# Kernel tuning notes

Measured on AMD Instinct MI355X. Metric: run time of the kernel, lower is better.

The kernel has to match this reference:

```python
import jax, jax.numpy as jnp
import numpy as np

HID = 64

def setup_inputs() -> dict:
    key = jax.random.key(0)
    ks = jax.random.split(key, 32)
    Nc, Na, B = 65536, 8192, 128
    Ecc, Eca, Eac, Eaa = 1048576, 262144, 262144, 131072
    d = {}
    d['x_context'] = jax.random.normal(ks[0], (Nc, 2), jnp.float32)
    d['x_action'] = jax.random.normal(ks[1], (Na, 2), jnp.float32)
    d['timestep'] = jax.random.randint(ks[2], (B,), 0, 1000)
    d['batch_idx'] = jax.random.randint(ks[3], (Na,), 0, B)
    d['cc_src'] = jax.random.randint(ks[4], (Ecc,), 0, Nc)
    d['cc_dst'] = jax.random.randint(ks[5], (Ecc,), 0, Nc)
    d['ca_src'] = jax.random.randint(ks[6], (Eca,), 0, Nc)
    d['ca_dst'] = jax.random.randint(ks[7], (Eca,), 0, Na)
    d['ac_src'] = jax.random.randint(ks[8], (Eac,), 0, Na)
    d['ac_dst'] = jax.random.randint(ks[9], (Eac,), 0, Nc)
    d['aa_src'] = jax.random.randint(ks[10], (Eaa,), 0, Na)
    d['aa_dst'] = jax.random.randint(ks[11], (Eaa,), 0, Na)
    def w(k, shape, fan_in):
        return jax.random.normal(k, shape, jnp.float32) / np.sqrt(fan_in)
    # input embeddings
    d['W_ctx'] = w(ks[12], (2, HID), 2); d['b_ctx'] = jnp.zeros((HID,), jnp.float32)
    d['W_act'] = w(ks[13], (2, HID), 2); d['b_act'] = jnp.zeros((HID,), jnp.float32)
    # time MLP
    d['tW1'] = w(ks[14], (HID, 2 * HID), HID); d['tb1'] = jnp.zeros((2 * HID,), jnp.float32)
    d['tW2'] = w(ks[15], (2 * HID, HID), 2 * HID); d['tb2'] = jnp.zeros((HID,), jnp.float32)
    # 2 SAGE layers, 4 edge types each (stacked: [cc, ca, ac, aa])
    d['c1_Wl'] = w(ks[16], (4, HID, HID), HID); d['c1_bl'] = jnp.zeros((4, HID), jnp.float32)
    d['c1_Wr'] = w(ks[17], (4, HID, HID), HID)
    d['c2_Wl'] = w(ks[18], (4, HID, HID), HID); d['c2_bl'] = jnp.zeros((4, HID), jnp.float32)
    d['c2_Wr'] = w(ks[19], (4, HID, HID), HID)
    # noise predictor
    d['nW1'] = w(ks[20], (2 * HID, HID), 2 * HID); d['nb1'] = jnp.zeros((HID,), jnp.float32)
    d['nW2'] = w(ks[21], (HID, 2), HID); d['nb2'] = jnp.zeros((2,), jnp.float32)
    return d


def _sage(x_src, x_dst, src, dst, Wl, bl, Wr):
    # PyG SAGEConv: lin_l(mean of neighbor msgs) + lin_r(self)
    n_dst = x_dst.shape[0]
    s = jax.ops.segment_sum(x_src[src], dst, num_segments=n_dst)
    cnt = jax.ops.segment_sum(jnp.ones((src.shape[0], 1), x_src.dtype), dst, num_segments=n_dst)
    mean = s / jnp.maximum(cnt, 1.0)
    return mean @ Wl + bl + x_dst @ Wr


def reference(x_context, x_action, timestep, batch_idx, cc_src, cc_dst, ca_src, ca_dst, ac_src, ac_dst, aa_src, aa_dst, W_ctx, b_ctx, W_act, b_act, tW1, tb1, tW2, tb2, c1_Wl, c1_bl, c1_Wr, c2_Wl, c2_bl, c2_Wr, nW1, nb1, nW2, nb2):
    h_ctx = x_context @ W_ctx + b_ctx           # [Nc, H]
    h_act = x_action @ W_act + b_act            # [Na, H]
    # hetero SAGE layer 1 (aggr='sum' over edge types per dst node type)
    o_ctx = (_sage(h_ctx, h_ctx, cc_src, cc_dst, c1_Wl[0], c1_bl[0], c1_Wr[0])
             + _sage(h_act, h_ctx, ac_src, ac_dst, c1_Wl[2], c1_bl[2], c1_Wr[2]))
    o_act = (_sage(h_ctx, h_act, ca_src, ca_dst, c1_Wl[1], c1_bl[1], c1_Wr[1])
             + _sage(h_act, h_act, aa_src, aa_dst, c1_Wl[3], c1_bl[3], c1_Wr[3]))
    h_ctx, h_act = jax.nn.relu(o_ctx), jax.nn.relu(o_act)
    # hetero SAGE layer 2
    o_act = (_sage(h_ctx, h_act, ca_src, ca_dst, c2_Wl[1], c2_bl[1], c2_Wr[1])
             + _sage(h_act, h_act, aa_src, aa_dst, c2_Wl[3], c2_bl[3], c2_Wr[3]))
    action_features = o_act                      # [Na, H]
    # sinusoidal time embedding + MLP
    half = HID // 2
    freqs = jnp.exp(-jnp.log(10000.0) * jnp.arange(half, dtype=jnp.float32) / (half - 1))
    ang = timestep.astype(jnp.float32)[:, None] * freqs[None, :]
    temb = jnp.concatenate([jnp.sin(ang), jnp.cos(ang)], axis=-1)   # [B, H]
    temb = jax.nn.gelu(temb @ tW1 + tb1, approximate=False) @ tW2 + tb2
    # gather per-node time embedding, fuse, predict noise
    fused = jnp.concatenate([action_features, temb[batch_idx]], axis=-1)  # [Na, 2H]
    h = jax.nn.gelu(fused @ nW1 + nb1, approximate=False)
    return h @ nW2 + nb2                         # [Na, node_features]
```

## Files before the change

### kernel.cpp

```cpp
#include <hip/hip_runtime.h>
#include <math.h>

#define HID 64
#define SLOTS 8192
#define WCC 40
#define WAC 10
#define NSCAT 64
#define CAP_CA 112
#define CAP_AA 80

__device__ __forceinline__ float gelu_exact(float x) {
    return 0.5f * x * (1.0f + erff(x * 0.70710678118654752f));
}

__device__ __forceinline__ float bf2f(unsigned short u) {
    return __uint_as_float(((unsigned int)u) << 16);
}
__device__ __forceinline__ unsigned short f2bf(float x) {
    unsigned int b = __float_as_uint(x);
    b += 0x7FFFu + ((b >> 16) & 1u);
    return (unsigned short)(b >> 16);
}

#define FXS 32768.0f
#define FXB (1 << 19)

__device__ __forceinline__ unsigned long long pack_edge(float2 v) {
    unsigned int f0 = (unsigned int)(__float2int_rn(v.x * FXS) + FXB);
    unsigned int f1 = (unsigned int)(__float2int_rn(v.y * FXS) + FXB);
    return (1ULL << 52) | ((unsigned long long)f1 << 26) | f0;
}

__device__ __forceinline__ void decode_acc(unsigned long long A, float& s0, float& s1, float& c) {
    int cnt = (int)(A >> 52);
    long long f0 = (long long)(A & 0x3FFFFFFULL) - (long long)cnt * FXB;
    long long f1 = (long long)((A >> 26) & 0x3FFFFFFULL) - (long long)cnt * FXB;
    s0 = (float)f0 * (1.0f / FXS);
    s1 = (float)f1 * (1.0f / FXS);
    c = (float)cnt;
}

__global__ __launch_bounds__(1024) void mega_kernel(
    const float* __restrict__ W_ctx, const float* __restrict__ b_ctx,
    const float* __restrict__ W_act, const float* __restrict__ b_act,
    const float* __restrict__ c1_Wl, const float* __restrict__ c1_bl,
    const float* __restrict__ c1_Wr,
    const float* __restrict__ c2_Wr, const float* __restrict__ c2_bl,
    float* __restrict__ P,
    const int* __restrict__ timestep,
    const float* __restrict__ tW1, const float* __restrict__ tb1,
    const float* __restrict__ tW2, const float* __restrict__ tb2,
    float* __restrict__ temb, int B,
    const int* __restrict__ cc_src, const int* __restrict__ cc_dst,
    const float* __restrict__ x_ctx, unsigned long long* __restrict__ pcc,
    int Ecc, int perCC,
    const int* __restrict__ ac_src, const int* __restrict__ ac_dst,
    const float* __restrict__ x_act, unsigned long long* __restrict__ pac,
    int Eac, int perAC,
    const int* __restrict__ ca_src, const int* __restrict__ ca_dst, int Eca,
    const int* __restrict__ aa_src, const int* __restrict__ aa_dst, int Eaa,
    int* __restrict__ cur_ca, int* __restrict__ csr_ca,
    int* __restrict__ cur_aa, int* __restrict__ csr_aa,
    int Nc, int bCC, int bAC, int bSC) {
    __shared__ unsigned long long slab[SLOTS];
    int blk = blockIdx.x;
    int tid = threadIdx.x;

    if (blk == 0) {
        if (tid < 64) {
            int j = tid;
            float a0, a1, c;

            a0 = a1 = c = 0.f;
            for (int k = 0; k < 64; k++) {
                float l = c1_Wr[k * 64 + j] + c1_Wr[2 * 4096 + k * 64 + j];
                a0 += W_ctx[k] * l; a1 += W_ctx[64 + k] * l; c += b_ctx[k] * l;
            }
            P[j] = a0; P[64 + j] = a1; P[128 + j] = c + c1_bl[j] + c1_bl[128 + j];

            a0 = a1 = c = 0.f;
            for (int k = 0; k < 64; k++) {
                float l = c1_Wl[k * 64 + j];
                a0 += W_ctx[k] * l; a1 += W_ctx[64 + k] * l; c += b_ctx[k] * l;
            }
            P[192 + j] = a0; P[256 + j] = a1; P[320 + j] = c;

            a0 = a1 = c = 0.f;
            for (int k = 0; k < 64; k++) {
                float l = c1_Wl[2 * 4096 + k * 64 + j];
                a0 += W_act[k] * l; a1 += W_act[64 + k] * l; c += b_act[k] * l;
            }
            P[384 + j] = a0; P[448 + j] = a1; P[512 + j] = c;

            a0 = a1 = c = 0.f;
            for (int k = 0; k < 64; k++) {
                float l = c1_Wr[4096 + k * 64 + j] + c1_Wr[3 * 4096 + k * 64 + j];
                a0 += W_act[k] * l; a1 += W_act[64 + k] * l; c += b_act[k] * l;
            }
            P[576 + j] = a0; P[640 + j] = a1; P[704 + j] = c + c1_bl[64 + j] + c1_bl[192 + j];

            a0 = a1 = c = 0.f;
            for (int k = 0; k < 64; k++) {
                float l = c1_Wl[4096 + k * 64 + j];
                a0 += W_ctx[k] * l; a1 += W_ctx[64 + k] * l; c += b_ctx[k] * l;
            }
            P[768 + j] = a0; P[832 + j] = a1; P[896 + j] = c;

            a0 = a1 = c = 0.f;
            for (int k = 0; k < 64; k++) {
                float l = c1_Wl[3 * 4096 + k * 64 + j];
                a0 += W_act[k] * l; a1 += W_act[64 + k] * l; c += b_act[k] * l;
            }
            P[960 + j] = a0; P[1024 + j] = a1; P[1088 + j] = c;

            for (int k = 0; k < 64; k++)
                P[1152 + k * 64 + j] = c2_Wr[4096 + k * 64 + j] + c2_Wr[3 * 4096 + k * 64 + j];
            P[5248 + j] = c2_bl[64 + j] + c2_bl[192 + j];
        }
    } else if (blk < bCC) {
        float* fl = (float*)slab;
        int sub = tid >> 7;
        int t = tid & 127;
        int b = (blk - 1) * 8 + sub;
        bool vb = (b < B);
        float* e = fl + sub * 64;
        float* t1 = fl + 512 + sub * 128;
        float ts = vb ? (float)timestep[b] : 0.f;
        if (t < 64) {
            int jj = t & 31;
            float f = expf(-9.210340371976184f * (float)jj / 31.0f);
            float ang = ts * f;
            e[t] = (t < 32) ? sinf(ang) : cosf(ang);
        }
        __syncthreads();
        {
            float a = tb1[t];
            #pragma unroll 8
            for (int k = 0; k < 64; k++) a += e[k] * tW1[k * 128 + t];
            t1[t] = gelu_exact(a);
        }
        __syncthreads();
        if (t < 64 && vb) {
            float a = tb2[t];
            #pragma unroll 8
            for (int k = 0; k < 128; k++) a += t1[k] * tW2[k * 64 + t];
            temb[b * 64 + t] = a;
        }
    } else if (blk < bAC) {
        int q = blk - bCC;
        int r = q / WCC, s = q % WCC;
        for (int k = tid; k < SLOTS; k += 1024) slab[k] = 0;
        __syncthreads();
        int lo = r * SLOTS;
        int e0 = s * perCC;
        int e1 = min(e0 + perCC, Ecc);
        const float2* xc2 = (const float2*)x_ctx;
        for (int e = e0 + tid * 4; e < e1; e += 4096) {
            int4 d4 = *(const int4*)(cc_dst + e);
            int4 s4 = *(const int4*)(cc_src + e);
            unsigned int o0 = (unsigned int)(d4.x - lo);
            unsigned int o1 = (unsigned int)(d4.y - lo);
            unsigned int o2 = (unsigned int)(d4.z - lo);
            unsigned int o3 = (unsigned int)(d4.w - lo);
            if (o0 < SLOTS) atomicAdd(&slab[o0], pack_edge(xc2[s4.x]));
            if (o1 < SLOTS) atomicAdd(&slab[o1], pack_edge(xc2[s4.y]));
            if (o2 < SLOTS) atomicAdd(&slab[o2], pack_edge(xc2[s4.z]));
            if (o3 < SLOTS) atomicAdd(&slab[o3], pack_edge(xc2[s4.w]));
        }
        __syncthreads();
        for (int k = tid; k < SLOTS; k += 1024)
            pcc[(size_t)s * Nc + lo + k] = slab[k];
    } else if (blk < bSC) {
        int q = blk - bAC;
        int r = q / WAC, s = q % WAC;
        for (int k = tid; k < SLOTS; k += 1024) slab[k] = 0;
        __syncthreads();
        int lo = r * SLOTS;
        int e0 = s * perAC;
        int e1 = min(e0 + perAC, Eac);
        const float2* xa2 = (const float2*)x_act;
        for (int e = e0 + tid * 4; e < e1; e += 4096) {
            int4 d4 = *(const int4*)(ac_dst + e);
            int4 s4 = *(const int4*)(ac_src + e);
            unsigned int o0 = (unsigned int)(d4.x - lo);
            unsigned int o1 = (unsigned int)(d4.y - lo);
            unsigned int o2 = (unsigned int)(d4.z - lo);
            unsigned int o3 = (unsigned int)(d4.w - lo);
            if (o0 < SLOTS) atomicAdd(&slab[o0], pack_edge(xa2[s4.x]));
            if (o1 < SLOTS) atomicAdd(&slab[o1], pack_edge(xa2[s4.y]));
            if (o2 < SLOTS) atomicAdd(&slab[o2], pack_edge(xa2[s4.z]));
            if (o3 < SLOTS) atomicAdd(&slab[o3], pack_edge(xa2[s4.w]));
        }
        __syncthreads();
        for (int k = tid; k < SLOTS; k += 1024)
            pac[(size_t)s * Nc + lo + k] = slab[k];
    } else {
        int tot = Eca + Eaa;
        for (int e = (blk - bSC) * 1024 + tid; e < tot; e += NSCAT * 1024) {
            if (e < Eca) {
                int d = ca_dst[e];
                int pos = atomicAdd(&cur_ca[d], 1);
                if (pos < CAP_CA) csr_ca[d * CAP_CA + pos] = ca_src[e];
            } else {
                int e2 = e - Eca;
                int d = aa_dst[e2];
                int pos = atomicAdd(&cur_aa[d], 1);
                if (pos < CAP_AA) csr_aa[d * CAP_AA + pos] = aa_src[e2];
            }
        }
    }
}

__global__ void mid_kernel(const unsigned long long* __restrict__ pcc,
                           const unsigned long long* __restrict__ pac,
                           const float* __restrict__ x_ctx, const float* __restrict__ x_act,
                           const float* __restrict__ P,
                           const int* __restrict__ cur_ca, const int* __restrict__ csr_ca,
                           const int* __restrict__ cur_aa, const int* __restrict__ csr_aa,
                           unsigned short* __restrict__ hb_ctx,
                           unsigned short* __restrict__ hb_act,
                           int Nc, int Na, int Gctx) {
    int blk = blockIdx.x;
    if (blk < Gctx) {
        __shared__ float nd[256][8];
        int t = threadIdx.x;
        int i = blk * 256 + t;
        if (i < Nc) {
            unsigned long long A = 0, Bv = 0;
            #pragma unroll
            for (int s = 0; s < WCC; s++) A += pcc[(size_t)s * Nc + i];
            #pragma unroll
            for (int s = 0; s < WAC; s++) Bv += pac[(size_t)s * Nc + i];
            float s0, s1, cc, a0, a1, ca;
            decode_acc(A, s0, s1, cc);
            decode_acc(Bv, a0, a1, ca);
            float2 xv = ((const float2*)x_ctx)[i];
            float rcc = 1.f / fmaxf(cc, 1.f), rac = 1.f / fmaxf(ca, 1.f);
            nd[t][0] = s0 * rcc; nd[t][1] = s1 * rcc; nd[t][2] = (cc > 0.f) ? 1.f : 0.f;
            nd[t][3] = a0 * rac; nd[t][4] = a1 * rac; nd[t][5] = (ca > 0.f) ? 1.f : 0.f;
            nd[t][6] = xv.x; nd[t][7] = xv.y;
        }
        __syncthreads();
        int t2 = threadIdx.x;
        int ns = t2 >> 6, j = t2 & 63;
        float p0 = P[j], p1 = P[64 + j], p2 = P[128 + j];
        float p3 = P[192 + j], p4 = P[256 + j], p5 = P[320 + j];
        float p6 = P[384 + j], p7 = P[448 + j], p8 = P[512 + j];
        for (int it = 0; it < 64; it++) {
            int ln = it * 4 + ns;
            int gi = blk * 256 + ln;
            if (gi >= Nc) break;
            float o = nd[ln][6] * p0 + nd[ln][7] * p1 + p2
                    + nd[ln][0] * p3 + nd[ln][1] * p4 + nd[ln][2] * p5
                    + nd[ln][3] * p6 + nd[ln][4] * p7 + nd[ln][5] * p8;
            hb_ctx[(size_t)gi * 64 + j] = f2bf(fmaxf(o, 0.f));
        }
    } else {
        int n = threadIdx.x >> 6, lane = threadIdx.x & 63;
        int i = (blk - Gctx) * 4 + n;
        if (i >= Na) return;
        const float2* xc2 = (const float2*)x_ctx;
        const float2* xa2 = (const float2*)x_act;
        int m_ca = cur_ca[i], it_ca = min(m_ca, CAP_CA);
        int b0 = i * CAP_CA;
        float s0 = 0.f, s1 = 0.f;
        for (int k = lane; k < it_ca; k += 64) { float2 v = xc2[csr_ca[b0 + k]]; s0 += v.x; s1 += v.y; }
        int m_aa = cur_aa[i], it_aa = min(m_aa, CAP_AA);
        int b1 = i * CAP_AA;
        float a0 = 0.f, a1 = 0.f;
        for (int k = lane; k < it_aa; k += 64) { float2 v = xa2[csr_aa[b1 + k]]; a0 += v.x; a1 += v.y; }
        for (int off = 32; off; off >>= 1) {
            s0 += __shfl_xor(s0, off); s1 += __shfl_xor(s1, off);
            a0 += __shfl_xor(a0, off); a1 += __shfl_xor(a1, off);
        }
        float cca = (float)m_ca, caa = (float)m_aa;
        float rca = 1.f / fmaxf(cca, 1.f), raa = 1.f / fmaxf(caa, 1.f);
        float m0 = s0 * rca, m1 = s1 * rca, q0 = a0 * raa, q1 = a1 * raa;
        float2 xa = xa2[i];
        int j = lane;
        float o = xa.x * P[576 + j] + xa.y * P[640 + j] + P[704 + j]
                + m0 * P[768 + j] + m1 * P[832 + j] + (cca > 0.f ? P[896 + j] : 0.f)
                + q0 * P[960 + j] + q1 * P[1024 + j] + (caa > 0.f ? P[1088 + j] : 0.f);
        hb_act[(size_t)i * 64 + j] = f2bf(fmaxf(o, 0.f));
    }
}

__global__ void act_l2_head_kernel(const unsigned short* __restrict__ hb_ctx,
                                   const unsigned short* __restrict__ hb_act,
                                   const int* __restrict__ cur_ca, const int* __restrict__ csr_ca,
                                   const int* __restrict__ cur_aa, const int* __restrict__ csr_aa,
                                   const float* __restrict__ c2_Wl, const float* __restrict__ P,
                                   const float* __restrict__ temb, const int* __restrict__ batch_idx,
                                   const float* __restrict__ nW1, const float* __restrict__ nb1,
                                   const float* __restrict__ nW2, const float* __restrict__ nb2,
                                   float* __restrict__ out, int N) {
    int n = threadIdx.x >> 6;
    int l = threadIdx.x & 63;
    int half = l >> 5;
    int c2 = l & 31;
    int i = blockIdx.x * 4 + n;
    bool act = (i < N);
    __shared__ float smca[4][64], smaa[4][64], shr[4][64], sfused[4][128], sh1[4][64];

    const unsigned int* hc32 = (const unsigned int*)hb_ctx;
    const unsigned int* ha32 = (const unsigned int*)hb_act;

    if (act) {
        int m = cur_ca[i], mi = min(m, CAP_CA);
        int b = i * CAP_CA;
        float s0 = 0.f, s1 = 0.f;
        #pragma unroll 4
        for (int k = half; k < mi; k += 2) {
            unsigned int w = hc32[(size_t)csr_ca[b + k] * 32 + c2];
            s0 += bf2f((unsigned short)(w & 0xFFFFu));
            s1 += bf2f((unsigned short)(w >> 16));
        }
        s0 += __shfl_xor(s0, 32);
        s1 += __shfl_xor(s1, 32);
        float rm = 1.f / fmaxf((float)m, 1.f);
        if (half == 0) { smca[n][c2 * 2] = s0 * rm; smca[n][c2 * 2 + 1] = s1 * rm; }

        m = cur_aa[i]; mi = min(m, CAP_AA);
        b = i * CAP_AA;
        s0 = 0.f; s1 = 0.f;
        #pragma unroll 4
        for (int k = half; k < mi; k += 2) {
            unsigned int w = ha32[(size_t)csr_aa[b + k] * 32 + c2];
            s0 += bf2f((unsigned short)(w & 0xFFFFu));
            s1 += bf2f((unsigned short)(w >> 16));
        }
        s0 += __shfl_xor(s0, 32);
        s1 += __shfl_xor(s1, 32);
        rm = 1.f / fmaxf((float)m, 1.f);
        if (half == 0) { smaa[n][c2 * 2] = s0 * rm; smaa[n][c2 * 2 + 1] = s1 * rm; }

        shr[n][l] = bf2f(hb_act[(size_t)i * 64 + l]);
    }
    __syncthreads();

    if (act) {
        const float* Wl1  = c2_Wl + 4096;
        const float* Wl3  = c2_Wl + 3 * 4096;
        const float* Wr2s = P + 1152;
        float o = P[5248 + l];
        #pragma unroll 8
        for (int k = 0; k < 64; k++) {
            o += smca[n][k] * Wl1[k * 64 + l]
               + smaa[n][k] * Wl3[k * 64 + l]
               + shr[n][k]  * Wr2s[k * 64 + l];
        }
        sfused[n][l] = o;
        sfused[n][64 + l] = temb[(size_t)batch_idx[i] * 64 + l];
    }
    __syncthreads();

    if (act) {
        float h = nb1[l];
        #pragma unroll 8
        for (int k = 0; k < 128; k++) h += sfused[n][k] * nW1[k * 64 + l];
        sh1[n][l] = gelu_exact(h);
    }
    __syncthreads();

    if (act && l < 2) {
        float v = nb2[l];
        #pragma unroll 8
        for (int k = 0; k < 64; k++) v += sh1[n][k] * nW2[k * 2 + l];
        out[(size_t)i * 2 + l] = v;
    }
}

extern "C" void kernel_launch(void* const* d_in, const int* in_sizes, int n_in,
                              void* d_out, int out_size, void* d_ws, size_t ws_size,
                              hipStream_t stream) {
    const float* x_context = (const float*)d_in[0];
    const float* x_action  = (const float*)d_in[1];
    const int*   timestep  = (const int*)d_in[2];
    const int*   batch_idx = (const int*)d_in[3];
    const int*   cc_src = (const int*)d_in[4];
    const int*   cc_dst = (const int*)d_in[5];
    const int*   ca_src = (const int*)d_in[6];
    const int*   ca_dst = (const int*)d_in[7];
    const int*   ac_src = (const int*)d_in[8];
    const int*   ac_dst = (const int*)d_in[9];
    const int*   aa_src = (const int*)d_in[10];
    const int*   aa_dst = (const int*)d_in[11];
    const float* W_ctx = (const float*)d_in[12];
    const float* b_ctx = (const float*)d_in[13];
    const float* W_act = (const float*)d_in[14];
    const float* b_act = (const float*)d_in[15];
    const float* tW1 = (const float*)d_in[16];
    const float* tb1 = (const float*)d_in[17];
    const float* tW2 = (const float*)d_in[18];
    const float* tb2 = (const float*)d_in[19];
    const float* c1_Wl = (const float*)d_in[20];
    const float* c1_bl = (const float*)d_in[21];
    const float* c1_Wr = (const float*)d_in[22];
    const float* c2_Wl = (const float*)d_in[23];
    const float* c2_bl = (const float*)d_in[24];
    const float* c2_Wr = (const float*)d_in[25];
    const float* nW1 = (const float*)d_in[26];
    const float* nb1 = (const float*)d_in[27];
    const float* nW2 = (const float*)d_in[28];
    const float* nb2 = (const float*)d_in[29];
    float* out = (float*)d_out;

    const int Nc  = in_sizes[0] / 2;
    const int Na  = in_sizes[1] / 2;
    const int B   = in_sizes[2];
    const int Ecc = in_sizes[4];
    const int Eca = in_sizes[6];
    const int Eac = in_sizes[8];
    const int Eaa = in_sizes[10];

    char* ws = (char*)d_ws;
    size_t o = 0;
    unsigned long long* pcc = (unsigned long long*)(ws + o); o += (size_t)WCC * Nc * 8;
    unsigned long long* pac = (unsigned long long*)(ws + o); o += (size_t)WAC * Nc * 8;
    int* cur_ca = (int*)(ws + o); o += (size_t)Na * 4;
    int* cur_aa = (int*)(ws + o); o += (size_t)Na * 4;
    int* csr_ca = (int*)(ws + o); o += (size_t)Na * CAP_CA * 4;
    int* csr_aa = (int*)(ws + o); o += (size_t)Na * CAP_AA * 4;
    float* P    = (float*)(ws + o); o += 8192 * 4;
    float* temb = (float*)(ws + o); o += (size_t)B * 64 * 4;
    unsigned short* hb_ctx = (unsigned short*)(ws + o); o += (size_t)Nc * 64 * 2;
    unsigned short* hb_act = (unsigned short*)(ws + o); o += (size_t)Na * 64 * 2;
    if (o > ws_size) return;

    hipMemsetAsync(cur_ca, 0, (size_t)Na * 8, stream);

    int RNG = (Nc + SLOTS - 1) / SLOTS;
    int nT  = (B + 7) / 8;
    int bCC = 1 + nT;
    int bAC = bCC + RNG * WCC;
    int bSC = bAC + RNG * WAC;
    int G   = bSC + NSCAT;
    int perCC = (((Ecc + WCC - 1) / WCC) + 3) & ~3;
    int perAC = (((Eac + WAC - 1) / WAC) + 3) & ~3;

    mega_kernel<<<G, 1024, 0, stream>>>(
        W_ctx, b_ctx, W_act, b_act, c1_Wl, c1_bl, c1_Wr, c2_Wr, c2_bl, P,
        timestep, tW1, tb1, tW2, tb2, temb, B,
        cc_src, cc_dst, x_context, pcc, Ecc, perCC,
        ac_src, ac_dst, x_action, pac, Eac, perAC,
        ca_src, ca_dst, Eca, aa_src, aa_dst, Eaa,
        cur_ca, csr_ca, cur_aa, csr_aa,
        Nc, bCC, bAC, bSC);

    int Gctx = (Nc + 255) / 256;
    int Gact = (Na + 3) / 4;
    mid_kernel<<<Gctx + Gact, 256, 0, stream>>>(
        pcc, pac, x_context, x_action, P,
        cur_ca, csr_ca, cur_aa, csr_aa, hb_ctx, hb_act, Nc, Na, Gctx);

    act_l2_head_kernel<<<(Na + 3) / 4, 256, 0, stream>>>(
        hb_ctx, hb_act, cur_ca, csr_ca, cur_aa, csr_aa,
        c2_Wl, P, temb, batch_idx, nW1, nb1, nW2, nb2, out, Na);
}
```

Baseline: 92.19 us.

## Build CSR via shared-memory histograms and prefix offsets instead of global atomics

Replaces the global-atomic CSR fill for ca/aa edges with a three-pass scheme: per-slice shared-memory histograms, a per-destination prefix over slices, then a shared-atomic scatter. Action-node layer-1 mean aggregation is moved from CSR gathers to packed fixed-point shared-memory scatter slabs, the same path already used for context nodes. cc/ac scatter loops skip loading source indices when none of the four destinations fall in the block's range, and WCC drops from 40 to 32. This removes the memset and contended global atomics but adds an extra kernel launch and another pass over the edge lists.

```diff
diff --git a/kernel.cpp b/kernel.cpp
--- a/kernel.cpp
+++ b/kernel.cpp
@@ -3,9 +3,12 @@
 
 #define HID 64
 #define SLOTS 8192
-#define WCC 40
+#define WCC 32
 #define WAC 10
-#define NSCAT 64
+#define SCA 8
+#define SAA 4
+#define HCA 16
+#define HAA 8
 #define CAP_CA 112
 #define CAP_AA 80
 
@@ -40,7 +43,7 @@
     c = (float)cnt;
 }
 
-__global__ __launch_bounds__(1024) void mega_kernel(
+__global__ __launch_bounds__(1024) void k1_kernel(
     const float* __restrict__ W_ctx, const float* __restrict__ b_ctx,
     const float* __restrict__ W_act, const float* __restrict__ b_act,
     const float* __restrict__ c1_Wl, const float* __restrict__ c1_bl,
@@ -59,9 +62,9 @@
     int Eac, int perAC,
     const int* __restrict__ ca_src, const int* __restrict__ ca_dst, int Eca,
     const int* __restrict__ aa_src, const int* __restrict__ aa_dst, int Eaa,
-    int* __restrict__ cur_ca, int* __restrict__ csr_ca,
-    int* __restrict__ cur_aa, int* __restrict__ csr_aa,
-    int Nc, int bCC, int bAC, int bSC) {
+    unsigned long long* __restrict__ pca, unsigned long long* __restrict__ paa,
+    int* __restrict__ hca, int* __restrict__ haa,
+    int Nc, int bCC, int bAC, int bXA, int bXB, int bHA, int bHB) {
     __shared__ unsigned long long slab[SLOTS];
     int blk = blockIdx.x;
     int tid = threadIdx.x;
@@ -124,7 +127,7 @@
         int b = (blk - 1) * 8 + sub;
         bool vb = (b < B);
         float* e = fl + sub * 64;
-        float* t1 = fl + 512 + sub * 128;
+        float* t1 = fl + 2048 + sub * 128;
         float ts = vb ? (float)timestep[b] : 0.f;
         if (t < 64) {
             int jj = t & 31;
@@ -157,20 +160,22 @@
         const float2* xc2 = (const float2*)x_ctx;
         for (int e = e0 + tid * 4; e < e1; e += 4096) {
             int4 d4 = *(const int4*)(cc_dst + e);
-            int4 s4 = *(const int4*)(cc_src + e);
             unsigned int o0 = (unsigned int)(d4.x - lo);
             unsigned int o1 = (unsigned int)(d4.y - lo);
             unsigned int o2 = (unsigned int)(d4.z - lo);
             unsigned int o3 = (unsigned int)(d4.w - lo);
-            if (o0 < SLOTS) atomicAdd(&slab[o0], pack_edge(xc2[s4.x]));
-            if (o1 < SLOTS) atomicAdd(&slab[o1], pack_edge(xc2[s4.y]));
-            if (o2 < SLOTS) atomicAdd(&slab[o2], pack_edge(xc2[s4.z]));
-            if (o3 < SLOTS) atomicAdd(&slab[o3], pack_edge(xc2[s4.w]));
+            if ((o0 < SLOTS) | (o1 < SLOTS) | (o2 < SLOTS) | (o3 < SLOTS)) {
+                int4 s4 = *(const int4*)(cc_src + e);
+                if (o0 < SLOTS) atomicAdd(&slab[o0], pack_edge(xc2[s4.x]));
+                if (o1 < SLOTS) atomicAdd(&slab[o1], pack_edge(xc2[s4.y]));
+                if (o2 < SLOTS) atomicAdd(&slab[o2], pack_edge(xc2[s4.z]));
+                if (o3 < SLOTS) atomicAdd(&slab[o3], pack_edge(xc2[s4.w]));
+            }
         }
         __syncthreads();
         for (int k = tid; k < SLOTS; k += 1024)
             pcc[(size_t)s * Nc + lo + k] = slab[k];
-    } else if (blk < bSC) {
+    } else if (blk < bXA) {
         int q = blk - bAC;
         int r = q / WAC, s = q % WAC;
         for (int k = tid; k < SLOTS; k += 1024) slab[k] = 0;
@@ -181,53 +186,166 @@
         const float2* xa2 = (const float2*)x_act;
         for (int e = e0 + tid * 4; e < e1; e += 4096) {
             int4 d4 = *(const int4*)(ac_dst + e);
-            int4 s4 = *(const int4*)(ac_src + e);
             unsigned int o0 = (unsigned int)(d4.x - lo);
             unsigned int o1 = (unsigned int)(d4.y - lo);
             unsigned int o2 = (unsigned int)(d4.z - lo);
             unsigned int o3 = (unsigned int)(d4.w - lo);
-            if (o0 < SLOTS) atomicAdd(&slab[o0], pack_edge(xa2[s4.x]));
-            if (o1 < SLOTS) atomicAdd(&slab[o1], pack_edge(xa2[s4.y]));
-            if (o2 < SLOTS) atomicAdd(&slab[o2], pack_edge(xa2[s4.z]));
-            if (o3 < SLOTS) atomicAdd(&slab[o3], pack_edge(xa2[s4.w]));
+            if ((o0 < SLOTS) | (o1 < SLOTS) | (o2 < SLOTS) | (o3 < SLOTS)) {
+                int4 s4 = *(const int4*)(ac_src + e);
+                if (o0 < SLOTS) atomicAdd(&slab[o0], pack_edge(xa2[s4.x]));
+                if (o1 < SLOTS) atomicAdd(&slab[o1], pack_edge(xa2[s4.y]));
+                if (o2 < SLOTS) atomicAdd(&slab[o2], pack_edge(xa2[s4.z]));
+                if (o3 < SLOTS) atomicAdd(&slab[o3], pack_edge(xa2[s4.w]));
+            }
         }
         __syncthreads();
         for (int k = tid; k < SLOTS; k += 1024)
             pac[(size_t)s * Nc + lo + k] = slab[k];
+    } else if (blk < bXB) {
+        int s = blk - bXA;
+        for (int k = tid; k < SLOTS; k += 1024) slab[k] = 0;
+        __syncthreads();
+        int per = (Eca + SCA - 1) / SCA;
+        int e0 = s * per, e1 = min(e0 + per, Eca);
+        const float2* xc2 = (const float2*)x_ctx;
+        for (int e = e0 + tid * 4; e < e1; e += 4096) {
+            int4 d4 = *(const int4*)(ca_dst + e);
+            int4 s4 = *(const int4*)(ca_src + e);
+            atomicAdd(&slab[d4.x], pack_edge(xc2[s4.x]));
+            atomicAdd(&slab[d4.y], pack_edge(xc2[s4.y]));
+            atomicAdd(&slab[d4.z], pack_edge(xc2[s4.z]));
+            atomicAdd(&slab[d4.w], pack_edge(xc2[s4.w]));
+        }
+        __syncthreads();
+        for (int k = tid; k < SLOTS; k += 1024)
+            pca[(size_t)s * SLOTS + k] = slab[k];
+    } else if (blk < bHA) {
+        int s = blk - bXB;
+        for (int k = tid; k < SLOTS; k += 1024) slab[k] = 0;
+        __syncthreads();
+        int per = (Eaa + SAA - 1) / SAA;
+        int e0 = s * per, e1 = min(e0 + per, Eaa);
+        const float2* xa2 = (const float2*)x_act;
+        for (int e = e0 + tid * 4; e < e1; e += 4096) {
+            int4 d4 = *(const int4*)(aa_dst + e);
+            int4 s4 = *(const int4*)(aa_src + e);
+            atomicAdd(&slab[d4.x], pack_edge(xa2[s4.x]));
+            atomicAdd(&slab[d4.y], pack_edge(xa2[s4.y]));
+            atomicAdd(&slab[d4.z], pack_edge(xa2[s4.z]));
+            atomicAdd(&slab[d4.w], pack_edge(xa2[s4.w]));
+        }
+        __syncthreads();
+        for (int k = tid; k < SLOTS; k += 1024)
+            paa[(size_t)s * SLOTS + k] = slab[k];
+    } else if (blk < bHB) {
+        int s = blk - bHA;
+        int* hist = (int*)slab;
+        for (int k = tid; k < SLOTS; k += 1024) hist[k] = 0;
+        __syncthreads();
+        int per = (Eca + HCA - 1) / HCA;
+        int e0 = s * per, e1 = min(e0 + per, Eca);
+        for (int e = e0 + tid * 4; e < e1; e += 4096) {
+            int4 d4 = *(const int4*)(ca_dst + e);
+            atomicAdd(&hist[d4.x], 1); atomicAdd(&hist[d4.y], 1);
+            atomicAdd(&hist[d4.z], 1); atomicAdd(&hist[d4.w], 1);
+        }
+        __syncthreads();
+        for (int k = tid; k < SLOTS; k += 1024) hca[s * SLOTS + k] = hist[k];
     } else {
-        int tot = Eca + Eaa;
-        for (int e = (blk - bSC) * 1024 + tid; e < tot; e += NSCAT * 1024) {
-            if (e < Eca) {
-                int d = ca_dst[e];
-                int pos = atomicAdd(&cur_ca[d], 1);
-                if (pos < CAP_CA) csr_ca[d * CAP_CA + pos] = ca_src[e];
-            } else {
-                int e2 = e - Eca;
-                int d = aa_dst[e2];
-                int pos = atomicAdd(&cur_aa[d], 1);
-                if (pos < CAP_AA) csr_aa[d * CAP_AA + pos] = aa_src[e2];
-            }
-        }
-    }
-}
-
-__global__ void mid_kernel(const unsigned long long* __restrict__ pcc,
-                           const unsigned long long* __restrict__ pac,
-                           const float* __restrict__ x_ctx, const float* __restrict__ x_act,
-                           const float* __restrict__ P,
-                           const int* __restrict__ cur_ca, const int* __restrict__ csr_ca,
-                           const int* __restrict__ cur_aa, const int* __restrict__ csr_aa,
-                           unsigned short* __restrict__ hb_ctx,
-                           unsigned short* __restrict__ hb_act,
-                           int Nc, int Na, int Gctx) {
+        int s = blk - bHB;
+        int* hist = (int*)slab;
+        for (int k = tid; k < SLOTS; k += 1024) hist[k] = 0;
+        __syncthreads();
+        int per = (Eaa + HAA - 1) / HAA;
+        int e0 = s * per, e1 = min(e0 + per, Eaa);
+        for (int e = e0 + tid * 4; e < e1; e += 4096) {
+            int4 d4 = *(const int4*)(aa_dst + e);
+            atomicAdd(&hist[d4.x], 1); atomicAdd(&hist[d4.y], 1);
+            atomicAdd(&hist[d4.z], 1); atomicAdd(&hist[d4.w], 1);
+        }
+        __syncthreads();
+        for (int k = tid; k < SLOTS; k += 1024) haa[s * SLOTS + k] = hist[k];
+    }
+}
+
+__global__ void k2_kernel(int* __restrict__ hca, int* __restrict__ haa,
+                          int* __restrict__ cnt_ca, int* __restrict__ cnt_aa) {
+    int d = blockIdx.x * 1024 + threadIdx.x;
+    int run = 0;
+    #pragma unroll
+    for (int s = 0; s < HCA; s++) {
+        int h = hca[s * SLOTS + d];
+        hca[s * SLOTS + d] = run;
+        run += h;
+    }
+    cnt_ca[d] = run;
+    run = 0;
+    #pragma unroll
+    for (int s = 0; s < HAA; s++) {
+        int h = haa[s * SLOTS + d];
+        haa[s * SLOTS + d] = run;
+        run += h;
+    }
+    cnt_aa[d] = run;
+}
+
+__global__ __launch_bounds__(1024) void k3_kernel(
+    const int* __restrict__ ca_src, const int* __restrict__ ca_dst, int Eca,
+    const int* __restrict__ aa_src, const int* __restrict__ aa_dst, int Eaa,
+    const int* __restrict__ hca, const int* __restrict__ haa,
+    int* __restrict__ csr_ca, int* __restrict__ csr_aa,
+    const unsigned long long* __restrict__ pcc, const unsigned long long* __restrict__ pac,
+    const unsigned long long* __restrict__ pca, const unsigned long long* __restrict__ paa,
+    const float* __restrict__ x_ctx, const float* __restrict__ x_act,
+    const float* __restrict__ P,
+    unsigned short* __restrict__ hb_ctx, unsigned short* __restrict__ hb_act,
+    int Nc, int Na, int bCTX, int bACT) {
+    __shared__ int sh[SLOTS];
     int blk = blockIdx.x;
-    if (blk < Gctx) {
-        __shared__ float nd[256][8];
-        int t = threadIdx.x;
-        int i = blk * 256 + t;
+    int tid = threadIdx.x;
+
+    if (blk < HCA) {
+        int s = blk;
+        for (int k = tid; k < SLOTS; k += 1024) sh[k] = hca[s * SLOTS + k];
+        __syncthreads();
+        int per = (Eca + HCA - 1) / HCA;
+        int e0 = s * per, e1 = min(e0 + per, Eca);
+        for (int e = e0 + tid * 4; e < e1; e += 4096) {
+            int4 d4 = *(const int4*)(ca_dst + e);
+            int4 s4 = *(const int4*)(ca_src + e);
+            int p0 = atomicAdd(&sh[d4.x], 1);
+            int p1 = atomicAdd(&sh[d4.y], 1);
+            int p2 = atomicAdd(&sh[d4.z], 1);
+            int p3 = atomicAdd(&sh[d4.w], 1);
+            if (p0 < CAP_CA) csr_ca[d4.x * CAP_CA + p0] = s4.x;
+            if (p1 < CAP_CA) csr_ca[d4.y * CAP_CA + p1] = s4.y;
+            if (p2 < CAP_CA) csr_ca[d4.z * CAP_CA + p2] = s4.z;
+            if (p3 < CAP_CA) csr_ca[d4.w * CAP_CA + p3] = s4.w;
+        }
+    } else if (blk < bCTX) {
+        int s = blk - HCA;
+        for (int k = tid; k < SLOTS; k += 1024) sh[k] = haa[s * SLOTS + k];
+        __syncthreads();
+        int per = (Eaa + HAA - 1) / HAA;
+        int e0 = s * per, e1 = min(e0 + per, Eaa);
+        for (int e = e0 + tid * 4; e < e1; e += 4096) {
+            int4 d4 = *(const int4*)(aa_dst + e);
+            int4 s4 = *(const int4*)(aa_src + e);
+            int p0 = atomicAdd(&sh[d4.x], 1);
+            int p1 = atomicAdd(&sh[d4.y], 1);
+            int p2 = atomicAdd(&sh[d4.z], 1);
+            int p3 = atomicAdd(&sh[d4.w], 1);
+            if (p0 < CAP_AA) csr_aa[d4.x * CAP_AA + p0] = s4.x;
+            if (p1 < CAP_AA) csr_aa[d4.y * CAP_AA + p1] = s4.y;
+            if (p2 < CAP_AA) csr_aa[d4.z * CAP_AA + p2] = s4.z;
+            if (p3 < CAP_AA) csr_aa[d4.w * CAP_AA + p3] = s4.w;
+        }
+    } else if (blk < bACT) {
+        float (*nd)[8] = (float(*)[8])sh;
+        int i = (blk - bCTX) * 1024 + tid;
         if (i < Nc) {
             unsigned long long A = 0, Bv = 0;
-            #pragma unroll
+            #pragma unroll 8
             for (int s = 0; s < WCC; s++) A += pcc[(size_t)s * Nc + i];
             #pragma unroll
             for (int s = 0; s < WAC; s++) Bv += pac[(size_t)s * Nc + i];
@@ -236,19 +354,18 @@
             decode_acc(Bv, a0, a1, ca);
             float2 xv = ((const float2*)x_ctx)[i];
             float rcc = 1.f / fmaxf(cc, 1.f), rac = 1.f / fmaxf(ca, 1.f);
-            nd[t][0] = s0 * rcc; nd[t][1] = s1 * rcc; nd[t][2] = (cc > 0.f) ? 1.f : 0.f;
-            nd[t][3] = a0 * rac; nd[t][4] = a1 * rac; nd[t][5] = (ca > 0.f) ? 1.f : 0.f;
-            nd[t][6] = xv.x; nd[t][7] = xv.y;
-        }
-        __syncthreads();
-        int t2 = threadIdx.x;
-        int ns = t2 >> 6, j = t2 & 63;
+            nd[tid][0] = s0 * rcc; nd[tid][1] = s1 * rcc; nd[tid][2] = (cc > 0.f) ? 1.f : 0.f;
+            nd[tid][3] = a0 * rac; nd[tid][4] = a1 * rac; nd[tid][5] = (ca > 0.f) ? 1.f : 0.f;
+            nd[tid][6] = xv.x; nd[tid][7] = xv.y;
+        }
+        __syncthreads();
+        int ns = tid >> 6, j = tid & 63;
         float p0 = P[j], p1 = P[64 + j], p2 = P[128 + j];
         float p3 = P[192 + j], p4 = P[256 + j], p5 = P[320 + j];
         float p6 = P[384 + j], p7 = P[448 + j], p8 = P[512 + j];
         for (int it = 0; it < 64; it++) {
-            int ln = it * 4 + ns;
-            int gi = blk * 256 + ln;
+            int ln = it * 16 + ns;
+            int gi = (blk - bCTX) * 1024 + ln;
             if (gi >= Nc) break;
             float o = nd[ln][6] * p0 + nd[ln][7] * p1 + p2
                     + nd[ln][0] * p3 + nd[ln][1] * p4 + nd[ln][2] * p5
@@ -256,44 +373,49 @@
             hb_ctx[(size_t)gi * 64 + j] = f2bf(fmaxf(o, 0.f));
         }
     } else {
-        int n = threadIdx.x >> 6, lane = threadIdx.x & 63;
-        int i = (blk - Gctx) * 4 + n;
-        if (i >= Na) return;
-        const float2* xc2 = (const float2*)x_ctx;
-        const float2* xa2 = (const float2*)x_act;
-        int m_ca = cur_ca[i], it_ca = min(m_ca, CAP_CA);
-        int b0 = i * CAP_CA;
-        float s0 = 0.f, s1 = 0.f;
-        for (int k = lane; k < it_ca; k += 64) { float2 v = xc2[csr_ca[b0 + k]]; s0 += v.x; s1 += v.y; }
-        int m_aa = cur_aa[i], it_aa = min(m_aa, CAP_AA);
-        int b1 = i * CAP_AA;
-        float a0 = 0.f, a1 = 0.f;
-        for (int k = lane; k < it_aa; k += 64) { float2 v = xa2[csr_aa[b1 + k]]; a0 += v.x; a1 += v.y; }
-        for (int off = 32; off; off >>= 1) {
-            s0 += __shfl_xor(s0, off); s1 += __shfl_xor(s1, off);
-            a0 += __shfl_xor(a0, off); a1 += __shfl_xor(a1, off);
-        }
-        float cca = (float)m_ca, caa = (float)m_aa;
-        float rca = 1.f / fmaxf(cca, 1.f), raa = 1.f / fmaxf(caa, 1.f);
-        float m0 = s0 * rca, m1 = s1 * rca, q0 = a0 * raa, q1 = a1 * raa;
-        float2 xa = xa2[i];
-        int j = lane;
-        float o = xa.x * P[576 + j] + xa.y * P[640 + j] + P[704 + j]
-                + m0 * P[768 + j] + m1 * P[832 + j] + (cca > 0.f ? P[896 + j] : 0.f)
-                + q0 * P[960 + j] + q1 * P[1024 + j] + (caa > 0.f ? P[1088 + j] : 0.f);
-        hb_act[(size_t)i * 64 + j] = f2bf(fmaxf(o, 0.f));
-    }
-}
-
-__global__ void act_l2_head_kernel(const unsigned short* __restrict__ hb_ctx,
-                                   const unsigned short* __restrict__ hb_act,
-                                   const int* __restrict__ cur_ca, const int* __restrict__ csr_ca,
-                                   const int* __restrict__ cur_aa, const int* __restrict__ csr_aa,
-                                   const float* __restrict__ c2_Wl, const float* __restrict__ P,
-                                   const float* __restrict__ temb, const int* __restrict__ batch_idx,
-                                   const float* __restrict__ nW1, const float* __restrict__ nb1,
-                                   const float* __restrict__ nW2, const float* __restrict__ nb2,
-                                   float* __restrict__ out, int N) {
+        float (*nd)[8] = (float(*)[8])sh;
+        int i = (blk - bACT) * 1024 + tid;
+        if (i < Na) {
+            unsigned long long A = 0, Bv = 0;
+            #pragma unroll
+            for (int s = 0; s < SCA; s++) A += pca[(size_t)s * SLOTS + i];
+            #pragma unroll
+            for (int s = 0; s < SAA; s++) Bv += paa[(size_t)s * SLOTS + i];
+            float s0, s1, cc, a0, a1, ca;
+            decode_acc(A, s0, s1, cc);
+            decode_acc(Bv, a0, a1, ca);
+            float2 xv = ((const float2*)x_act)[i];
+            float rca = 1.f / fmaxf(cc, 1.f), raa = 1.f / fmaxf(ca, 1.f);
+            nd[tid][0] = s0 * rca; nd[tid][1] = s1 * rca; nd[tid][2] = (cc > 0.f) ? 1.f : 0.f;
+            nd[tid][3] = a0 * raa; nd[tid][4] = a1 * raa; nd[tid][5] = (ca > 0.f) ? 1.f : 0.f;
+            nd[tid][6] = xv.x; nd[tid][7] = xv.y;
+        }
+        __syncthreads();
+        int ns = tid >> 6, j = tid & 63;
+        float p0 = P[576 + j], p1 = P[640 + j], p2 = P[704 + j];
+        float p3 = P[768 + j], p4 = P[832 + j], p5 = P[896 + j];
+        float p6 = P[960 + j], p7 = P[1024 + j], p8 = P[1088 + j];
+        for (int it = 0; it < 64; it++) {
+            int ln = it * 16 + ns;
+            int gi = (blk - bACT) * 1024 + ln;
+            if (gi >= Na) break;
+            float o = nd[ln][6] * p0 + nd[ln][7] * p1 + p2
+                    + nd[ln][0] * p3 + nd[ln][1] * p4 + nd[ln][2] * p5
+                    + nd[ln][3] * p6 + nd[ln][4] * p7 + nd[ln][5] * p8;
+            hb_act[(size_t)gi * 64 + j] = f2bf(fmaxf(o, 0.f));
+        }
+    }
+}
+
+__global__ void k4_kernel(const unsigned short* __restrict__ hb_ctx,
+                          const unsigned short* __restrict__ hb_act,
+                          const int* __restrict__ cnt_ca, const int* __restrict__ csr_ca,
+                          const int* __restrict__ cnt_aa, const int* __restrict__ csr_aa,
+                          const float* __restrict__ c2_Wl, const float* __restrict__ P,
+                          const float* __restrict__ temb, const int* __restrict__ batch_idx,
+                          const float* __restrict__ nW1, const float* __restrict__ nb1,
+                          const float* __restrict__ nW2, const float* __restrict__ nb2,
+                          float* __restrict__ out, int N) {
     int n = threadIdx.x >> 6;
     int l = threadIdx.x & 63;
     int half = l >> 5;
@@ -306,7 +428,7 @@
     const unsigned int* ha32 = (const unsigned int*)hb_act;
 
     if (act) {
-        int m = cur_ca[i], mi = min(m, CAP_CA);
+        int m = cnt_ca[i], mi = min(m, CAP_CA);
         int b = i * CAP_CA;
         float s0 = 0.f, s1 = 0.f;
         #pragma unroll 4
@@ -320,7 +442,7 @@
         float rm = 1.f / fmaxf((float)m, 1.f);
         if (half == 0) { smca[n][c2 * 2] = s0 * rm; smca[n][c2 * 2 + 1] = s1 * rm; }
 
-        m = cur_aa[i]; mi = min(m, CAP_AA);
+        m = cnt_aa[i]; mi = min(m, CAP_AA);
         b = i * CAP_AA;
         s0 = 0.f; s1 = 0.f;
         #pragma unroll 4
@@ -417,8 +539,12 @@
     size_t o = 0;
     unsigned long long* pcc = (unsigned long long*)(ws + o); o += (size_t)WCC * Nc * 8;
     unsigned long long* pac = (unsigned long long*)(ws + o); o += (size_t)WAC * Nc * 8;
-    int* cur_ca = (int*)(ws + o); o += (size_t)Na * 4;
-    int* cur_aa = (int*)(ws + o); o += (size_t)Na * 4;
+    unsigned long long* pca = (unsigned long long*)(ws + o); o += (size_t)SCA * SLOTS * 8;
+    unsigned long long* paa = (unsigned long long*)(ws + o); o += (size_t)SAA * SLOTS * 8;
+    int* hca    = (int*)(ws + o); o += (size_t)HCA * SLOTS * 4;
+    int* haa    = (int*)(ws + o); o += (size_t)HAA * SLOTS * 4;
+    int* cnt_ca = (int*)(ws + o); o += (size_t)Na * 4;
+    int* cnt_aa = (int*)(ws + o); o += (size_t)Na * 4;
     int* csr_ca = (int*)(ws + o); o += (size_t)Na * CAP_CA * 4;
     int* csr_aa = (int*)(ws + o); o += (size_t)Na * CAP_AA * 4;
     float* P    = (float*)(ws + o); o += 8192 * 4;
@@ -427,33 +553,41 @@
     unsigned short* hb_act = (unsigned short*)(ws + o); o += (size_t)Na * 64 * 2;
     if (o > ws_size) return;
 
-    hipMemsetAsync(cur_ca, 0, (size_t)Na * 8, stream);
-
-    int RNG = (Nc + SLOTS - 1) / SLOTS;
-    int nT  = (B + 7) / 8;
-    int bCC = 1 + nT;
-    int bAC = bCC + RNG * WCC;
-    int bSC = bAC + RNG * WAC;
-    int G   = bSC + NSCAT;
-    int perCC = (((Ecc + WCC - 1) / WCC) + 3) & ~3;
-    int perAC = (((Eac + WAC - 1) / WAC) + 3) & ~3;
-
-    mega_kernel<<<G, 1024, 0, stream>>>(
+    const int RNG = (Nc + SLOTS - 1) / SLOTS;
+    const int nT  = (B + 7) / 8;
+    const int bCC = 1 + nT;
+    const int bAC = bCC + RNG * WCC;
+    const int bXA = bAC + RNG * WAC;
+    const int bXB = bXA + SCA;
+    const int bHA = bXB + SAA;
+    const int bHB = bHA + HCA;
+    const int G1  = bHB + HAA;
+    const int perCC = (((Ecc + WCC - 1) / WCC) + 3) & ~3;
+    const int perAC = (((Eac + WAC - 1) / WAC) + 3) & ~3;
+
+    k1_kernel<<<G1, 1024, 0, stream>>>(
         W_ctx, b_ctx, W_act, b_act, c1_Wl, c1_bl, c1_Wr, c2_Wr, c2_bl, P,
         timestep, tW1, tb1, tW2, tb2, temb, B,
         cc_src, cc_dst, x_context, pcc, Ecc, perCC,
         ac_src, ac_dst, x_action, pac, Eac, perAC,
         ca_src, ca_dst, Eca, aa_src, aa_dst, Eaa,
-        cur_ca, csr_ca, cur_aa, csr_aa,
-        Nc, bCC, bAC, bSC);
-
-    int Gctx = (Nc + 255) / 256;
-    int Gact = (Na + 3) / 4;
-    mid_kernel<<<Gctx + Gact, 256, 0, stream>>>(
-        pcc, pac, x_context, x_action, P,
-        cur_ca, csr_ca, cur_aa, csr_aa, hb_ctx, hb_act, Nc, Na, Gctx);
-
-    act_l2_head_kernel<<<(Na + 3) / 4, 256, 0, stream>>>(
-        hb_ctx, hb_act, cur_ca, csr_ca, cur_aa, csr_aa,
+        pca, paa, hca, haa,
+        Nc, bCC, bAC, bXA, bXB, bHA, bHB);
+
+    k2_kernel<<<(Na + 1023) / 1024, 1024, 0, stream>>>(hca, haa, cnt_ca, cnt_aa);
+
+    const int bCTX = HCA + HAA;
+    const int GctxB = (Nc + 1023) / 1024;
+    const int bACT = bCTX + GctxB;
+    const int GactB = (Na + 1023) / 1024;
+    k3_kernel<<<bACT + GactB, 1024, 0, stream>>>(
+        ca_src, ca_dst, Eca, aa_src, aa_dst, Eaa,
+        hca, haa, csr_ca, csr_aa,
+        pcc, pac, pca, paa,
+        x_context, x_action, P, hb_ctx, hb_act,
+        Nc, Na, bCTX, bACT);
+
+    k4_kernel<<<(Na + 3) / 4, 256, 0, stream>>>(
+        hb_ctx, hb_act, cnt_ca, csr_ca, cnt_aa, csr_aa,
         c2_Wl, P, temb, batch_idx, nW1, nb1, nW2, nb2, out, Na);
 }
```

New measurement: 101.0 us. +9.5%, slower.
